# Kernel optimization log

Measured on AMD Instinct MI355X. Metric: run time of the kernel, lower is better.

Reference implementation:

```python
import jax, jax.numpy as jnp
import numpy as np

H = 16  # attention heads


def setup_inputs() -> dict:
    key = jax.random.key(0)
    k0, k1, k2 = jax.random.split(key, 3)
    B, T, C = 2, 2048, 1024
    x = jax.random.normal(k0, (B, T, C), dtype=jnp.float32)
    W_attn = jax.random.normal(k1, (3 * C, C), dtype=jnp.float32) * 0.02
    W_proj = jax.random.normal(k2, (C, C), dtype=jnp.float32) * 0.02
    b_proj = jnp.zeros((C,), dtype=jnp.float32)
    return {"x": x, "W_attn": W_attn, "W_proj": W_proj, "b_proj": b_proj}


def reference(x, W_attn, W_proj, b_proj):
    # Eval-mode (dropout = identity), rotational_embeddings=False, flash=False path.
    B, T, C = x.shape
    d = C // H
    qkv = jnp.einsum('btc,fc->btf', x, W_attn)          # [B,T,3C] fused QKV proj
    q, k, v = jnp.split(qkv, 3, axis=-1)
    # [B,T,C] -> [B,H,T,d]
    q = q.reshape(B, T, H, d).transpose(0, 2, 1, 3)
    k = k.reshape(B, T, H, d).transpose(0, 2, 1, 3)
    v = v.reshape(B, T, H, d).transpose(0, 2, 1, 3)
    scale = 1.0 / np.sqrt(d).astype(np.float32)
    att = jnp.einsum('bhqd,bhkd->bhqk', q, k) * scale    # full TxT scores (no mask)
    att = jax.nn.softmax(att, axis=-1)
    y = jnp.einsum('bhqk,bhkd->bhqd', att, v)            # [B,H,T,d]
    y = y.transpose(0, 2, 1, 3).reshape(B, T, C)
    return jnp.einsum('btc,oc->bto', y, W_proj) + b_proj
```

## Files before the change

### kernel.cpp

```cpp
#include <hip/hip_runtime.h>
#include <hip/hip_bf16.h>
#include <stdint.h>

typedef __attribute__((ext_vector_type(8))) short bf16x8;
typedef __attribute__((ext_vector_type(4))) float f32x4;

#define MFMA16(A,B,C) __builtin_amdgcn_mfma_f32_16x16x32_bf16(A,B,C,0,0,0)


__device__ inline void gld_lds16(const __hip_bfloat16* g, __hip_bfloat16* l) {
  __builtin_amdgcn_global_load_lds(
      (const __attribute__((address_space(1))) void*)g,
      (__attribute__((address_space(3))) void*)l, 16, 0, 0);
}

__global__ __launch_bounds__(256)
void cvt_bf16(const float* __restrict__ s0, __hip_bfloat16* __restrict__ d0, int n0,
              const float* __restrict__ s1, __hip_bfloat16* __restrict__ d1, int n1,
              const float* __restrict__ s2, __hip_bfloat16* __restrict__ d2, int n2)
{
  const float* s; __hip_bfloat16* d; int n;
  if      (blockIdx.y == 0) { s = s0; d = d0; n = n0; }
  else if (blockIdx.y == 1) { s = s1; d = d1; n = n1; }
  else                      { s = s2; d = d2; n = n2; }
  int idx = (blockIdx.x * 256 + threadIdx.x) * 8;
  if (idx >= n) return;
  float4 u0 = *(const float4*)(s + idx);
  float4 u1 = *(const float4*)(s + idx + 4);
  __hip_bfloat16 t[8];
  t[0] = __float2bfloat16(u0.x); t[1] = __float2bfloat16(u0.y);
  t[2] = __float2bfloat16(u0.z); t[3] = __float2bfloat16(u0.w);
  t[4] = __float2bfloat16(u1.x); t[5] = __float2bfloat16(u1.y);
  t[6] = __float2bfloat16(u1.z); t[7] = __float2bfloat16(u1.w);
  *(int4*)(d + idx) = *(const int4*)t;
}

template<int BM, int BN, typename TC>
__global__ __launch_bounds__(256)
void gemm_bt(const __hip_bfloat16* __restrict__ A,
             const __hip_bfloat16* __restrict__ B,
             TC* __restrict__ C,
             const float* __restrict__ bias,
             __hip_bfloat16* __restrict__ vtg,
             int M, int N, int K)
{
  constexpr int MI = BM / 32;
  constexpr int NJ = BN / 32;
  constexpr int NP = (BM + BN) / 64;

  __shared__ __align__(16) __hip_bfloat16 As[BM * 32];
  __shared__ __align__(16) __hip_bfloat16 Bs[BN * 32];

  const int tid  = threadIdx.x;
  const int lane = tid & 63;
  const int w    = tid >> 6;
  const int lm   = lane & 15;
  const int g    = lane >> 4;

  const int bm = blockIdx.y * BM;
  const int bn = blockIdx.x * BN;
  const int rm = (w >> 1) * (BM / 2);
  const int cn = (w & 1) * (BN / 2);

  const f32x4 fzero = {0.0f, 0.0f, 0.0f, 0.0f};
  f32x4 acc[MI][NJ];
  for (int i = 0; i < MI; i++)
    for (int j = 0; j < NJ; j++)
      acc[i][j] = fzero;

  for (int k0 = 0; k0 < K; k0 += 32) {
    __syncthreads();
#pragma unroll
    for (int p = 0; p < NP; p++) {
      int c = tid + p * 256;
      if (c < BM * 4)
        gld_lds16(&A[(size_t)(bm + (c >> 2)) * K + k0 + (c & 3) * 8], &As[c * 8]);
      else {
        int cb = c - BM * 4;
        gld_lds16(&B[(size_t)(bn + (cb >> 2)) * K + k0 + (cb & 3) * 8], &Bs[cb * 8]);
      }
    }
    __syncthreads();

    bf16x8 af[MI], bfr[NJ];
#pragma unroll
    for (int i = 0; i < MI; i++)
      af[i] = *(const bf16x8*)&As[(rm + 16 * i + lm) * 32 + 8 * g];
#pragma unroll
    for (int j = 0; j < NJ; j++)
      bfr[j] = *(const bf16x8*)&Bs[(cn + 16 * j + lm) * 32 + 8 * g];
#pragma unroll
    for (int i = 0; i < MI; i++)
#pragma unroll
      for (int j = 0; j < NJ; j++)
        acc[i][j] = MFMA16(af[i], bfr[j], acc[i][j]);
  }

  if (vtg != nullptr && bn >= 2048) {
#pragma unroll
    for (int j = 0; j < NJ; j++) {
      int colv = bn + cn + 16 * j + lm - 2048;
      int vh = colv >> 6, dd = colv & 63;
#pragma unroll
      for (int i = 0; i < MI; i++) {
        int m0 = bm + rm + 16 * i + 4 * g;
        int bb = m0 >> 11, t0 = m0 & 2047;
        __hip_bfloat16 t4[4];
#pragma unroll
        for (int r = 0; r < 4; r++) t4[r] = __float2bfloat16(acc[i][j][r]);
        *(int2*)&vtg[((size_t)(bb * 16 + vh) * 64 + dd) * 2048 + t0] =
            *(const int2*)t4;
      }
    }
    return;
  }

#pragma unroll
  for (int j = 0; j < NJ; j++) {
    int coln = bn + cn + 16 * j + lm;
    float bv = bias ? bias[coln] : 0.0f;
#pragma unroll
    for (int i = 0; i < MI; i++) {
#pragma unroll
      for (int r = 0; r < 4; r++) {
        int rowm = bm + rm + 16 * i + 4 * g + r;
        float v = acc[i][j][r] + bv;
        if constexpr (sizeof(TC) == 2)
          C[(size_t)rowm * N + coln] = __float2bfloat16(v);
        else
          C[(size_t)rowm * N + coln] = v;
      }
    }
  }
}

__global__ __launch_bounds__(256)
void mha(const __hip_bfloat16* __restrict__ qkv,
         const __hip_bfloat16* __restrict__ vtg,
         __hip_bfloat16* __restrict__ yout,
         __hip_bfloat16* __restrict__ po,
         float* __restrict__ pl,
         int nsteps)
{
  const int T = 2048, F = 3072, Cc = 1024;
  const int bh = blockIdx.x;
  const int b  = bh >> 4, h = bh & 15;
  const int qb0 = blockIdx.y * 128;
  const int z   = blockIdx.z;
  const int kvb = z * 64 * nsteps;

  const int tid  = threadIdx.x;
  const int lane = tid & 63;
  const int w    = tid >> 6;
  const int lm   = lane & 15;
  const int g    = lane >> 4;

  __shared__ __align__(16) __hip_bfloat16 Ks[2][64 * 64];
  __shared__ __align__(16) __hip_bfloat16 Vs[2][64 * 64];
  __shared__ __align__(16) __hip_bfloat16 Pld[4][32 * 72];

  const size_t rowbase = (size_t)b * T * F;
  const int hoff = h * 64;
  const __hip_bfloat16* Kbase = qkv + rowbase + 1024 + hoff;
  const __hip_bfloat16* Vtb   = vtg + (size_t)(b * 16 + h) * 64 * 2048;

  const int qw = qb0 + 32 * w;
  bf16x8 aq[2][2];
#pragma unroll
  for (int mt = 0; mt < 2; mt++)
#pragma unroll
    for (int kcq = 0; kcq < 2; kcq++)
      aq[mt][kcq] = *(const bf16x8*)
          &qkv[rowbase + (size_t)(qw + 16 * mt + lm) * F + hoff + 32 * kcq + 8 * g];

  const f32x4 fzero = {0.0f, 0.0f, 0.0f, 0.0f};
  f32x4 yacc[2][4];
  float lsum[2][4];
#pragma unroll
  for (int mt = 0; mt < 2; mt++) {
#pragma unroll
    for (int c = 0; c < 4; c++) yacc[mt][c] = fzero;
#pragma unroll
    for (int r = 0; r < 4; r++) lsum[mt][r] = 0.0f;
  }

  const int r0 = tid >> 3;
  const int sw = (tid & 7) ^ (r0 & 7);
  const int sx = lm & 7;

  gld_lds16(Kbase + (size_t)(kvb + r0)      * F + sw * 8, &Ks[0][tid * 8]);
  gld_lds16(Kbase + (size_t)(kvb + r0 + 32) * F + sw * 8, &Ks[0][(tid + 256) * 8]);
  gld_lds16(Vtb + (size_t)r0        * 2048 + kvb + sw * 8, &Vs[0][tid * 8]);
  gld_lds16(Vtb + (size_t)(r0 + 32) * 2048 + kvb + sw * 8, &Vs[0][(tid + 256) * 8]);

  for (int t = 0; t < nsteps; t++) {
    const int buf = t & 1;
    __syncthreads();
    if (t + 1 < nsteps) {
      const int kvn = kvb + (t + 1) * 64;
      gld_lds16(Kbase + (size_t)(kvn + r0)      * F + sw * 8, &Ks[buf ^ 1][tid * 8]);
      gld_lds16(Kbase + (size_t)(kvn + r0 + 32) * F + sw * 8, &Ks[buf ^ 1][(tid + 256) * 8]);
      gld_lds16(Vtb + (size_t)r0        * 2048 + kvn + sw * 8, &Vs[buf ^ 1][tid * 8]);
      gld_lds16(Vtb + (size_t)(r0 + 32) * 2048 + kvn + sw * 8, &Vs[buf ^ 1][(tid + 256) * 8]);
    }

    f32x4 s[2][4];
#pragma unroll
    for (int c2 = 0; c2 < 4; c2++) {
      bf16x8 bk0 = *(const bf16x8*)&Ks[buf][(16 * c2 + lm) * 64 + ((0 + g) ^ sx) * 8];
      bf16x8 bk1 = *(const bf16x8*)&Ks[buf][(16 * c2 + lm) * 64 + ((4 + g) ^ sx) * 8];
#pragma unroll
      for (int mt = 0; mt < 2; mt++) {
        s[mt][c2] = MFMA16(aq[mt][0], bk0, fzero);
        s[mt][c2] = MFMA16(aq[mt][1], bk1, s[mt][c2]);
      }
    }

#pragma unroll
    for (int mt = 0; mt < 2; mt++)
#pragma unroll
      for (int c = 0; c < 4; c++)
#pragma unroll
        for (int r = 0; r < 4; r++) {
          float p = __expf(s[mt][c][r] * 0.125f);
          lsum[mt][r] += p;
          Pld[w][(16 * mt + 4 * g + r) * 72 + 16 * c + lm] = __float2bfloat16(p);
        }

    bf16x8 ap[2][2];
#pragma unroll
    for (int mt = 0; mt < 2; mt++)
#pragma unroll
      for (int kcp = 0; kcp < 2; kcp++)
        ap[mt][kcp] = *(const bf16x8*)&Pld[w][(16 * mt + lm) * 72 + 32 * kcp + 8 * g];
#pragma unroll
    for (int c = 0; c < 4; c++) {
#pragma unroll
      for (int e = 0; e < 2; e++) {
        bf16x8 bv = *(const bf16x8*)&Vs[buf][(16 * c + lm) * 64 + ((4 * e + g) ^ sx) * 8];
#pragma unroll
        for (int mt = 0; mt < 2; mt++)
          yacc[mt][c] = MFMA16(ap[mt][e], bv, yacc[mt][c]);
      }
    }
  }

#pragma unroll
  for (int mt = 0; mt < 2; mt++) {
    float lred[4];
#pragma unroll
    for (int r = 0; r < 4; r++) {
      float ls = lsum[mt][r];
      ls += __shfl_xor(ls, 1);
      ls += __shfl_xor(ls, 2);
      ls += __shfl_xor(ls, 4);
      ls += __shfl_xor(ls, 8);
      lred[r] = ls;
    }
    if (yout != nullptr) {
#pragma unroll
      for (int c = 0; c < 4; c++)
#pragma unroll
        for (int r = 0; r < 4; r++) {
          int qrow = qw + 16 * mt + 4 * g + r;
          yout[(size_t)(b * T + qrow) * Cc + hoff + 16 * c + lm] =
              __float2bfloat16(yacc[mt][c][r] / lred[r]);
        }
    } else {
      __hip_bfloat16* pz = po + (size_t)z * 4096 * 1024;
      float* plz = pl + (size_t)z * 4096 * 16;
#pragma unroll
      for (int c = 0; c < 4; c++)
#pragma unroll
        for (int r = 0; r < 4; r++) {
          int qrow = qw + 16 * mt + 4 * g + r;
          pz[(size_t)(b * T + qrow) * Cc + hoff + 16 * c + lm] =
              __float2bfloat16(yacc[mt][c][r]);
        }
      if (lm == 0)
#pragma unroll
        for (int r = 0; r < 4; r++) {
          int qrow = qw + 16 * mt + 4 * g + r;
          plz[(b * T + qrow) * 16 + h] = lred[r];
        }
    }
  }
}

__global__ __launch_bounds__(256)
void combine(const __hip_bfloat16* __restrict__ po,
             const float* __restrict__ pl,
             __hip_bfloat16* __restrict__ y)
{
  int idx = (blockIdx.x * 256 + threadIdx.x) * 8;
  int row = idx >> 10, c = idx & 1023, h = c >> 6;
  float la = pl[row * 16 + h];
  float lb = pl[4096 * 16 + row * 16 + h];
  float rinv = 1.0f / (la + lb);
  const __hip_bfloat16* pa = po + idx;
  const __hip_bfloat16* pb = po + 4096 * 1024 + idx;
  __hip_bfloat16 t[8];
#pragma unroll
  for (int j = 0; j < 8; j++)
    t[j] = __float2bfloat16(
        (__bfloat162float(pa[j]) + __bfloat162float(pb[j])) * rinv);
  *(int4*)(y + idx) = *(const int4*)t;
}

extern "C" void kernel_launch(void* const* d_in, const int* in_sizes, int n_in,
                              void* d_out, int out_size, void* d_ws, size_t ws_size,
                              hipStream_t stream)
{
  const float* x  = (const float*)d_in[0];
  const float* Wa = (const float*)d_in[1];
  const float* Wp = (const float*)d_in[2];
  const float* bp = (const float*)d_in[3];
  float* out = (float*)d_out;

  const int BT = 4096, C = 1024, F3 = 3072;
  char* ws = (char*)d_ws;
  __hip_bfloat16* qkv  = (__hip_bfloat16*)ws;
  __hip_bfloat16* vtg  = (__hip_bfloat16*)(ws + 25165824);
  __hip_bfloat16* xbf  = (__hip_bfloat16*)(ws + 33554432);
  __hip_bfloat16* yb   = xbf;
  __hip_bfloat16* Wabf = (__hip_bfloat16*)(ws + 41943040);
  __hip_bfloat16* Wpbf = (__hip_bfloat16*)(ws + 48234496);
  __hip_bfloat16* Opar = (__hip_bfloat16*)(ws + 50331648);
  float*          lpar = (float*)(ws + 67108864);
  const size_t need_split = 67633152;

  cvt_bf16<<<dim3(2048, 3), 256, 0, stream>>>(
      x, xbf, BT * C, Wa, Wabf, F3 * C, Wp, Wpbf, C * C);
  gemm_bt<128, 128, __hip_bfloat16>
      <<<dim3(F3 / 128, BT / 128), 256, 0, stream>>>(xbf, Wabf, qkv, nullptr, vtg,
                                                     BT, F3, C);
  if (ws_size >= need_split) {
    mha<<<dim3(32, 16, 2), 256, 0, stream>>>(qkv, vtg, nullptr, Opar, lpar, 16);
    combine<<<dim3(BT * C / 2048), 256, 0, stream>>>(Opar, lpar, yb);
  } else {
    mha<<<dim3(32, 16, 1), 256, 0, stream>>>(qkv, vtg, yb, nullptr, nullptr, 32);
  }
  gemm_bt<64, 128, float>
      <<<dim3(C / 128, BT / 64), 256, 0, stream>>>(yb, Wpbf, out, bp, nullptr,
                                                   BT, C, C);
}
```

Baseline: 221.2 us.

## Halve attention KV tile to 32 and fold softmax scale into Q projection

The attention kernel now processes 32 keys per step instead of 64, with smaller K/V/P shared-memory buffers, a new swizzle for the 32-wide transposed V tile, and twice as many steps. The 1/sqrt(d) scale is applied to the Q columns in the QKV GEMM epilogue, which removes one multiply per score inside the exponent. Smaller LDS use may allow more resident blocks per CU and better latency hiding. In exchange there are more barriers and loop iterations per block, and fewer MFMAs between synchronisations.

```diff
diff --git a/kernel.cpp b/kernel.cpp
--- a/kernel.cpp
+++ b/kernel.cpp
@@ -115,6 +115,7 @@
     return;
   }
 
+  const float qs = (vtg != nullptr && bn < 1024) ? 0.125f : 1.0f;
 #pragma unroll
   for (int j = 0; j < NJ; j++) {
     int coln = bn + cn + 16 * j + lm;
@@ -124,7 +125,7 @@
 #pragma unroll
       for (int r = 0; r < 4; r++) {
         int rowm = bm + rm + 16 * i + 4 * g + r;
-        float v = acc[i][j][r] + bv;
+        float v = acc[i][j][r] * qs + bv;
         if constexpr (sizeof(TC) == 2)
           C[(size_t)rowm * N + coln] = __float2bfloat16(v);
         else
@@ -147,7 +148,7 @@
   const int b  = bh >> 4, h = bh & 15;
   const int qb0 = blockIdx.y * 128;
   const int z   = blockIdx.z;
-  const int kvb = z * 64 * nsteps;
+  const int kvb = z * 32 * nsteps;
 
   const int tid  = threadIdx.x;
   const int lane = tid & 63;
@@ -155,9 +156,9 @@
   const int lm   = lane & 15;
   const int g    = lane >> 4;
 
-  __shared__ __align__(16) __hip_bfloat16 Ks[2][64 * 64];
-  __shared__ __align__(16) __hip_bfloat16 Vs[2][64 * 64];
-  __shared__ __align__(16) __hip_bfloat16 Pld[4][32 * 72];
+  __shared__ __align__(16) __hip_bfloat16 Ks[2][32 * 64];
+  __shared__ __align__(16) __hip_bfloat16 Vs[2][64 * 32];
+  __shared__ __align__(16) __hip_bfloat16 Pld[4][32 * 40];
 
   const size_t rowbase = (size_t)b * T * F;
   const int hoff = h * 64;
@@ -184,31 +185,30 @@
     for (int r = 0; r < 4; r++) lsum[mt][r] = 0.0f;
   }
 
-  const int r0 = tid >> 3;
-  const int sw = (tid & 7) ^ (r0 & 7);
-  const int sx = lm & 7;
-
-  gld_lds16(Kbase + (size_t)(kvb + r0)      * F + sw * 8, &Ks[0][tid * 8]);
-  gld_lds16(Kbase + (size_t)(kvb + r0 + 32) * F + sw * 8, &Ks[0][(tid + 256) * 8]);
-  gld_lds16(Vtb + (size_t)r0        * 2048 + kvb + sw * 8, &Vs[0][tid * 8]);
-  gld_lds16(Vtb + (size_t)(r0 + 32) * 2048 + kvb + sw * 8, &Vs[0][(tid + 256) * 8]);
+  const int r0  = tid >> 3;
+  const int swK = (tid & 7) ^ (r0 & 7);
+  const int vdd = tid >> 2;
+  const int vk  = (tid & 3) ^ ((tid >> 3) & 3);
+  const int sxK = lm & 7;
+  const int sxV = (lm >> 1) & 3;
+
+  gld_lds16(Kbase + (size_t)(kvb + r0) * F + swK * 8, &Ks[0][tid * 8]);
+  gld_lds16(Vtb + (size_t)vdd * 2048 + kvb + vk * 8, &Vs[0][tid * 8]);
 
   for (int t = 0; t < nsteps; t++) {
     const int buf = t & 1;
     __syncthreads();
     if (t + 1 < nsteps) {
-      const int kvn = kvb + (t + 1) * 64;
-      gld_lds16(Kbase + (size_t)(kvn + r0)      * F + sw * 8, &Ks[buf ^ 1][tid * 8]);
-      gld_lds16(Kbase + (size_t)(kvn + r0 + 32) * F + sw * 8, &Ks[buf ^ 1][(tid + 256) * 8]);
-      gld_lds16(Vtb + (size_t)r0        * 2048 + kvn + sw * 8, &Vs[buf ^ 1][tid * 8]);
-      gld_lds16(Vtb + (size_t)(r0 + 32) * 2048 + kvn + sw * 8, &Vs[buf ^ 1][(tid + 256) * 8]);
-    }
-
-    f32x4 s[2][4];
-#pragma unroll
-    for (int c2 = 0; c2 < 4; c2++) {
-      bf16x8 bk0 = *(const bf16x8*)&Ks[buf][(16 * c2 + lm) * 64 + ((0 + g) ^ sx) * 8];
-      bf16x8 bk1 = *(const bf16x8*)&Ks[buf][(16 * c2 + lm) * 64 + ((4 + g) ^ sx) * 8];
+      const int kvn = kvb + (t + 1) * 32;
+      gld_lds16(Kbase + (size_t)(kvn + r0) * F + swK * 8, &Ks[buf ^ 1][tid * 8]);
+      gld_lds16(Vtb + (size_t)vdd * 2048 + kvn + vk * 8, &Vs[buf ^ 1][tid * 8]);
+    }
+
+    f32x4 s[2][2];
+#pragma unroll
+    for (int c2 = 0; c2 < 2; c2++) {
+      bf16x8 bk0 = *(const bf16x8*)&Ks[buf][(16 * c2 + lm) * 64 + ((0 + g) ^ sxK) * 8];
+      bf16x8 bk1 = *(const bf16x8*)&Ks[buf][(16 * c2 + lm) * 64 + ((4 + g) ^ sxK) * 8];
 #pragma unroll
       for (int mt = 0; mt < 2; mt++) {
         s[mt][c2] = MFMA16(aq[mt][0], bk0, fzero);
@@ -219,29 +219,24 @@
 #pragma unroll
     for (int mt = 0; mt < 2; mt++)
 #pragma unroll
-      for (int c = 0; c < 4; c++)
+      for (int c2 = 0; c2 < 2; c2++)
 #pragma unroll
         for (int r = 0; r < 4; r++) {
-          float p = __expf(s[mt][c][r] * 0.125f);
+          float p = __expf(s[mt][c2][r]);
           lsum[mt][r] += p;
-          Pld[w][(16 * mt + 4 * g + r) * 72 + 16 * c + lm] = __float2bfloat16(p);
+          Pld[w][(16 * mt + 4 * g + r) * 40 + 16 * c2 + lm] = __float2bfloat16(p);
         }
 
-    bf16x8 ap[2][2];
+    bf16x8 ap[2];
 #pragma unroll
     for (int mt = 0; mt < 2; mt++)
-#pragma unroll
-      for (int kcp = 0; kcp < 2; kcp++)
-        ap[mt][kcp] = *(const bf16x8*)&Pld[w][(16 * mt + lm) * 72 + 32 * kcp + 8 * g];
+      ap[mt] = *(const bf16x8*)&Pld[w][(16 * mt + lm) * 40 + 8 * g];
 #pragma unroll
     for (int c = 0; c < 4; c++) {
-#pragma unroll
-      for (int e = 0; e < 2; e++) {
-        bf16x8 bv = *(const bf16x8*)&Vs[buf][(16 * c + lm) * 64 + ((4 * e + g) ^ sx) * 8];
-#pragma unroll
-        for (int mt = 0; mt < 2; mt++)
-          yacc[mt][c] = MFMA16(ap[mt][e], bv, yacc[mt][c]);
-      }
+      bf16x8 bv = *(const bf16x8*)&Vs[buf][(16 * c + lm) * 32 + (g ^ sxV) * 8];
+#pragma unroll
+      for (int mt = 0; mt < 2; mt++)
+        yacc[mt][c] = MFMA16(ap[mt], bv, yacc[mt][c]);
     }
   }
 
@@ -335,10 +330,10 @@
       <<<dim3(F3 / 128, BT / 128), 256, 0, stream>>>(xbf, Wabf, qkv, nullptr, vtg,
                                                      BT, F3, C);
   if (ws_size >= need_split) {
-    mha<<<dim3(32, 16, 2), 256, 0, stream>>>(qkv, vtg, nullptr, Opar, lpar, 16);
+    mha<<<dim3(32, 16, 2), 256, 0, stream>>>(qkv, vtg, nullptr, Opar, lpar, 32);
     combine<<<dim3(BT * C / 2048), 256, 0, stream>>>(Opar, lpar, yb);
   } else {
-    mha<<<dim3(32, 16, 1), 256, 0, stream>>>(qkv, vtg, yb, nullptr, nullptr, 32);
+    mha<<<dim3(32, 16, 1), 256, 0, stream>>>(qkv, vtg, yb, nullptr, nullptr, 64);
   }
   gemm_bt<64, 128, float>
       <<<dim3(C / 128, BT / 64), 256, 0, stream>>>(yb, Wpbf, out, bp, nullptr,
```

New measurement: 209.1 us. -5.4%, faster.
